# Performance work log

Measured on AMD Instinct MI355X. Metric: run time of the kernel, lower is better.

The kernel has to match this reference:

```python
import jax, jax.numpy as jnp
import numpy as np
from jax import lax

VOCAB, EMB, HID, MAXD, NCLS = 50000, 512, 512, 1024, 20
S, B = 512, 64

def setup_inputs() -> dict:
    key = jax.random.key(0)
    ks = jax.random.split(key, 16)
    sc = 0.05
    return {
        "inp": jax.random.randint(ks[0], (S, B), 0, VOCAB),
        "emb_table": jax.random.normal(ks[1], (VOCAB, EMB), jnp.float32) * sc,
        "c_l0": jax.random.normal(ks[2], (HID,), jnp.float32) * sc,
        "c_r0": jax.random.normal(ks[3], (HID,), jnp.float32) * sc,
        "W_l": jax.random.normal(ks[4], (HID, HID), jnp.float32) * sc,
        "b_l": jnp.zeros((HID,), jnp.float32),
        "W_r": jax.random.normal(ks[5], (HID, HID), jnp.float32) * sc,
        "b_r": jnp.zeros((HID,), jnp.float32),
        "W_sl": jax.random.normal(ks[6], (HID, EMB), jnp.float32) * sc,
        "b_sl": jnp.zeros((HID,), jnp.float32),
        "W_sr": jax.random.normal(ks[7], (EMB, HID), jnp.float32) * sc,  # emb_dim==hid_dim required by source
        "b_sr": jnp.zeros((EMB,), jnp.float32),
        "W_max": jax.random.normal(ks[8], (MAXD, 2 * HID + EMB), jnp.float32) * sc,
        "b_max": jnp.zeros((MAXD,), jnp.float32),
        "W_doc": jax.random.normal(ks[9], (NCLS, MAXD), jnp.float32) * sc,
        "b_doc": jnp.zeros((NCLS,), jnp.float32),
    }

def reference(inp, emb_table, c_l0, c_r0, W_l, b_l, W_r, b_r,
              W_sl, b_sl, W_sr, b_sr, W_max, b_max, W_doc, b_doc):
    # inp: [S, B] int; emb: [S, B, E]
    emb = emb_table[inp]
    # precomputed per-token projections (done once, outside the recurrence)
    emb_ls = jnp.einsum('sbe,he->sbh', emb, W_sl) + b_sl  # [S,B,H]
    emb_rs = jnp.einsum('sbe,he->sbh', emb, W_sr) + b_sr  # [S,B,H]

    def step(W, b):
        def f(c, e):  # c: [B,H], e: [B,H]
            c = jnp.tanh(c @ W.T + b + e)
            return c, c
        return f

    batch = inp.shape[1]
    c_l_init = jnp.broadcast_to(c_l0, (batch, HID))
    c_r_init = jnp.broadcast_to(c_r0, (batch, HID))
    _, c_ls = lax.scan(step(W_l, b_l), c_l_init, emb_ls)          # [S,B,H] left-to-right
    _, c_rs_rev = lax.scan(step(W_r, b_r), c_r_init, emb_rs[::-1])  # scanned right-to-left
    c_rs = c_rs_rev[::-1]                                          # re-aligned to positions

    cat = jnp.concatenate([c_ls, emb, c_rs], axis=2)               # [S,B,2H+E]
    y = jnp.tanh(jnp.einsum('sbc,mc->sbm', cat, W_max) + b_max)    # [S,B,M]
    y_max = jnp.max(y, axis=0)                                     # [B,M] max-pool over seq
    logits = y_max @ W_doc.T + b_doc                               # [B,C]
    return jax.nn.log_softmax(logits, axis=-1)
```

## Files before the change

kernel.cpp:

```cpp
#include <hip/hip_runtime.h>
#include <hip/hip_bf16.h>
#include <cstdint>
#include <cstddef>

#define SS   512
#define BB   64
#define EMBD 512
#define HIDD 512
#define MAXD 1024
#define NCLS 20
#define KCAT 1536
#define ROWS (SS*BB)

__device__ __forceinline__ uint16_t f2bf(float f) {
  uint32_t u = __float_as_uint(f);
  uint32_t r = u + 0x7fffu + ((u >> 16) & 1u);
  return (uint16_t)(r >> 16);
}
__device__ __forceinline__ float bf2f(uint32_t h) {
  return __uint_as_float(h << 16);
}
__device__ __forceinline__ uint32_t pk2(float a, float b) {
  return (uint32_t)f2bf(a) | ((uint32_t)f2bf(b) << 16);
}

__device__ __forceinline__ float fast_tanh(float x) {
  float ax = __builtin_fabsf(x);
  float e  = __builtin_amdgcn_exp2f(ax * -2.885390081777927f);
  float r  = (1.f - e) * __builtin_amdgcn_rcpf(1.f + e);
  return __builtin_copysignf(r, x);
}

#if defined(__has_builtin)
#if __has_builtin(__builtin_amdgcn_fdot2_f32_bf16)
#define USE_BF16_DOT2 1
#endif
#endif

#ifdef USE_BF16_DOT2
typedef __bf16 bf16x2_t __attribute__((ext_vector_type(2)));
__device__ __forceinline__ float dot2bf(uint32_t w, uint32_t c, float acc) {
  return __builtin_amdgcn_fdot2_f32_bf16(__builtin_bit_cast(bf16x2_t, w),
                                         __builtin_bit_cast(bf16x2_t, c), acc, false);
}
#else
__device__ __forceinline__ float dot2bf(uint32_t w, uint32_t c, float acc) {
  float w0 = __uint_as_float(w << 16);
  float w1 = __uint_as_float(w & 0xffff0000u);
  float c0 = __uint_as_float(c << 16);
  float c1 = __uint_as_float(c & 0xffff0000u);
  return fmaf(w1, c1, fmaf(w0, c0, acc));
}
#endif

__device__ __forceinline__ void gl_lds16(const void* g, void* l) {
  __builtin_amdgcn_global_load_lds((const __attribute__((address_space(1))) void*)g,
                                   (__attribute__((address_space(3))) void*)l,
                                   16, 0, 0);
}

typedef short v8s __attribute__((ext_vector_type(8)));
typedef float v4f __attribute__((ext_vector_type(4)));

__global__ __launch_bounds__(256) void prep_kernel(
    const int* __restrict__ inp, const float* __restrict__ table,
    const float* __restrict__ Wsl, const float* __restrict__ Wsr,
    const float* __restrict__ Wl,  const float* __restrict__ Wr,
    const float* __restrict__ Wmax,
    uint16_t* __restrict__ cat, uint16_t* __restrict__ wslb,
    uint16_t* __restrict__ wsrb, uint16_t* __restrict__ wlb,
    uint16_t* __restrict__ wrb, uint16_t* __restrict__ wmaxb)
{
  const int blk = blockIdx.x, t = threadIdx.x;
  if (blk < 8192) {
    const int r = blk * 4 + (t >> 6);
    const int lane = t & 63;
    const int token = inp[r];
    const float4* src = (const float4*)(table + (size_t)token * EMBD);
    uint16_t* dst = cat + (size_t)r * KCAT + 512;
#pragma unroll
    for (int p = 0; p < 2; ++p) {
      const int slot = lane + 64 * p;
      float4 v = src[slot];
      uint2 o;
      o.x = pk2(v.x, v.y);
      o.y = pk2(v.z, v.w);
      *(uint2*)(dst + slot * 4) = o;
    }
  } else {
    size_t flat = (size_t)(blk - 8192) * 2048 + (size_t)t * 8;
    const float* src; uint16_t* dst; size_t off;
    if (flat < 262144)       { src = Wsl;  dst = wslb;  off = flat; }
    else if (flat < 524288)  { src = Wsr;  dst = wsrb;  off = flat - 262144; }
    else if (flat < 786432)  { src = Wl;   dst = wlb;   off = flat - 524288; }
    else if (flat < 1048576) { src = Wr;   dst = wrb;   off = flat - 786432; }
    else                     { src = Wmax; dst = wmaxb; off = flat - 1048576; }
    float4 v0 = *(const float4*)(src + off);
    float4 v1 = *(const float4*)(src + off + 4);
    uint4 o;
    o.x = pk2(v0.x, v0.y); o.y = pk2(v0.z, v0.w);
    o.z = pk2(v1.x, v1.y); o.w = pk2(v1.z, v1.w);
    *(uint4*)(dst + off) = o;
  }
}

template<int MODE>
__global__ __launch_bounds__(256, 2) void gemm_kernel(
    const uint16_t* __restrict__ A, int lda, int K,
    const uint16_t* __restrict__ W0, const uint16_t* __restrict__ W1,
    const float* __restrict__ bias0, const float* __restrict__ bias1,
    uint16_t* __restrict__ outb, float* __restrict__ partial)
{
  __shared__ unsigned char smem[32768];
  uint16_t* lA = (uint16_t*)smem;
  uint16_t* lW = (uint16_t*)(smem + 16384);

  const int tid = threadIdx.x;
  const int mb = blockIdx.x, nb = blockIdx.y;
  const int m0 = mb * 128, n0 = nb * 128;

  const uint16_t* Wp = W0;
  const float* biasp = bias0;
  int nr0 = n0;
  if (MODE == 0 && n0 >= 512) { Wp = W1; biasp = bias1; nr0 = n0 - 512; }

  const int w = tid >> 6, lane = tid & 63;
  const int mw = w & 1, nw = w >> 1;

  v4f acc[4][4];
#pragma unroll
  for (int i = 0; i < 4; ++i)
#pragma unroll
    for (int j = 0; j < 4; ++j) {
      v4f z = {0.f, 0.f, 0.f, 0.f};
      acc[i][j] = z;
    }

  const int r_st = tid >> 3;
  const int u_st = tid & 7;

  for (int kk = 0; kk < K; kk += 64) {
    __syncthreads();
#pragma unroll
    for (int p = 0; p < 4; ++p) {
      const int r = p * 32 + r_st;
      gl_lds16(A + (size_t)(m0 + r) * lda + kk + u_st * 8, lA + (p * 256 + tid) * 8);
    }
#pragma unroll
    for (int p = 0; p < 4; ++p) {
      const int r = p * 32 + r_st;
      gl_lds16(Wp + (size_t)(nr0 + r) * K + kk + u_st * 8, lW + (p * 256 + tid) * 8);
    }
    __syncthreads();
#pragma unroll
    for (int ks = 0; ks < 2; ++ks) {
      v8s af[4], wf[4];
#pragma unroll
      for (int i = 0; i < 4; ++i)
        af[i] = *(const v8s*)&lA[(mw * 64 + i * 16 + (lane & 15)) * 64 + ks * 32 + (lane >> 4) * 8];
#pragma unroll
      for (int j = 0; j < 4; ++j)
        wf[j] = *(const v8s*)&lW[(nw * 64 + j * 16 + (lane & 15)) * 64 + ks * 32 + (lane >> 4) * 8];
#pragma unroll
      for (int i = 0; i < 4; ++i)
#pragma unroll
        for (int j = 0; j < 4; ++j)
          acc[i][j] = __builtin_amdgcn_mfma_f32_16x16x32_bf16(af[i], wf[j], acc[i][j], 0, 0, 0);
    }
  }

  __syncthreads();

  if (MODE == 0) {
#pragma unroll
    for (int i = 0; i < 4; ++i)
#pragma unroll
      for (int j = 0; j < 4; ++j) {
        const int nl = nw * 64 + j * 16 + (lane & 15);
        const float bv = biasp[nr0 + nl];
        const int colg = n0 + nl;
#pragma unroll
        for (int r = 0; r < 4; ++r) {
          const int rowg = m0 + mw * 64 + i * 16 + (lane >> 4) * 4 + r;
          outb[(size_t)rowg * 1024 + colg] = f2bf(acc[i][j][r] + bv);
        }
      }
  } else {
    float* lred = (float*)smem;
    if (mw == 1) {
#pragma unroll
      for (int i = 0; i < 4; ++i)
#pragma unroll
        for (int j = 0; j < 4; ++j) {
          const int nl = nw * 64 + j * 16 + (lane & 15);
          const float bv = biasp[nr0 + nl];
#pragma unroll
          for (int r = 0; r < 4; ++r) {
            const int bl = i * 16 + (lane >> 4) * 4 + r;
            lred[bl * 128 + nl] = fast_tanh(acc[i][j][r] + bv);
          }
        }
    }
    __syncthreads();
    if (mw == 0) {
#pragma unroll
      for (int i = 0; i < 4; ++i)
#pragma unroll
        for (int j = 0; j < 4; ++j) {
          const int nl = nw * 64 + j * 16 + (lane & 15);
          const float bv = biasp[nr0 + nl];
#pragma unroll
          for (int r = 0; r < 4; ++r) {
            const int bl = i * 16 + (lane >> 4) * 4 + r;
            const float v = fast_tanh(acc[i][j][r] + bv);
            partial[((size_t)mb * 64 + bl) * 1024 + n0 + nl] = fmaxf(v, lred[bl * 128 + nl]);
          }
        }
    }
  }
}

__global__ __launch_bounds__(512, 1) void scan_kernel(
    const uint16_t* __restrict__ ee,
    const uint16_t* __restrict__ wlb, const uint16_t* __restrict__ wrb,
    const float* __restrict__ bl, const float* __restrict__ br,
    const float* __restrict__ cl0, const float* __restrict__ cr0,
    uint16_t* __restrict__ cat,
    uint64_t* __restrict__ cbuf)
{
  const int tid = threadIdx.x;
  const int bid = blockIdx.x;
  const int b    = bid & 63;
  const int d    = (bid >> 6) & 1;
  const int half = bid >> 7;

  const int hp = tid & 127;
  const int kq = tid >> 7;

  __shared__ __align__(16) uint32_t cfull[256];
  __shared__ float2 part2[4 * 128];

  uint4 wA[16], wB[16];
  {
    const uint16_t* wsrc = (d ? wrb : wlb) + (size_t)(half * 256 + 2 * hp) * HIDD + kq * 128;
    const uint4* pA = (const uint4*)wsrc;
    const uint4* pB = (const uint4*)(wsrc + HIDD);
#pragma unroll
    for (int j = 0; j < 16; ++j) { wA[j] = pA[j]; wB[j] = pB[j]; }
  }
  if (tid < 256) {
    const float* c0v = d ? cr0 : cl0;
    float2 cv = ((const float2*)c0v)[tid];
    cfull[tid] = pk2(cv.x, cv.y);
  }
  float2 biasv = {0.f, 0.f};
  if (tid < 128) {
    const float* bvec = d ? br : bl;
    biasv = ((const float2*)bvec)[half * 128 + tid];
  }
  __syncthreads();

  const int fp = tid;
  const size_t ecol = (size_t)(d * 512 + half * 256 + 2 * fp);
  const int fcol = (d ? 1024 : 0) + half * 256 + 2 * fp;

  const int gj = tid - 128;
  const int pbid = bid ^ 128;

  uint32_t ep0 = 0, ep1 = 0;
  if (tid < 128) {
    const int s0i = d ? 511 : 0;
    const int s1i = d ? 510 : 1;
    ep0 = *(const uint32_t*)&ee[(size_t)(s0i * BB + b) * 1024 + ecol];
    ep1 = *(const uint32_t*)&ee[(size_t)(s1i * BB + b) * 1024 + ecol];
  }

  uint32_t prPrev = 0;
  int sPrev = -1;

  for (int i = 0; i < 512; ++i) {
    const int s = d ? (511 - i) : i;
    uint32_t ep2 = 0;
    if (tid < 128) {
      const int i2 = (i + 2) & 511;
      const int s2 = d ? (511 - i2) : i2;
      ep2 = *(const uint32_t*)&ee[(size_t)(s2 * BB + b) * 1024 + ecol];
      if (sPrev >= 0)
        *(uint32_t*)&cat[(size_t)(sPrev * BB + b) * KCAT + fcol] = prPrev;
    }

    {
      const uint32_t* cb_ = &cfull[kq * 64];
      float a0 = 0.f, a1 = 0.f, a2 = 0.f, a3 = 0.f;
#pragma unroll
      for (int j = 0; j < 16; ++j) {
        uint4 c4 = *(const uint4*)(cb_ + j * 4);
        a0 = dot2bf(wA[j].x, c4.x, a0); a2 = dot2bf(wB[j].x, c4.x, a2);
        a1 = dot2bf(wA[j].y, c4.y, a1); a3 = dot2bf(wB[j].y, c4.y, a3);
        a0 = dot2bf(wA[j].z, c4.z, a0); a2 = dot2bf(wB[j].z, c4.z, a2);
        a1 = dot2bf(wA[j].w, c4.w, a1); a3 = dot2bf(wB[j].w, c4.w, a3);
      }
      float2 pv; pv.x = a0 + a1; pv.y = a2 + a3;
      part2[kq * 128 + hp] = pv;
    }

    const uint64_t want = (uint64_t)(uint32_t)(i + 1);
    const uint64_t* slot = &cbuf[(size_t)(((i & 1) * 256 + pbid) * 128 + gj)];
    uint64_t vprobe = 0;
    if (tid >= 128 && tid < 256 && i != 511)
      vprobe = __hip_atomic_load(slot, __ATOMIC_RELAXED, __HIP_MEMORY_SCOPE_AGENT);

    __syncthreads();

    if (tid < 128) {
      float2 q0 = part2[fp];
      float2 q1 = part2[128 + fp];
      float2 q2 = part2[256 + fp];
      float2 q3 = part2[384 + fp];
      float s0 = ((q0.x + q1.x) + (q2.x + q3.x)) + biasv.x + bf2f(ep0 & 0xffffu);
      float s1 = ((q0.y + q1.y) + (q2.y + q3.y)) + biasv.y + bf2f(ep0 >> 16);
      uint32_t pr = pk2(fast_tanh(s0), fast_tanh(s1));
      if (i != 511) {
        uint64_t pkt = (want << 32) | (uint64_t)pr;
        __hip_atomic_store(&cbuf[(size_t)(((i & 1) * 256 + bid) * 128 + fp)],
                           pkt, __ATOMIC_RELAXED, __HIP_MEMORY_SCOPE_AGENT);
        cfull[half * 128 + fp] = pr;
        prPrev = pr; sPrev = s;
      } else {
        *(uint32_t*)&cat[(size_t)(s * BB + b) * KCAT + fcol] = pr;
      }
    } else if (tid < 256 && i != 511) {
      uint64_t v = vprobe;
      while ((v >> 32) != want) {
        v = __hip_atomic_load(slot, __ATOMIC_RELAXED, __HIP_MEMORY_SCOPE_AGENT);
        if ((v >> 32) == want) break;
        __builtin_amdgcn_s_sleep(1);
        v = __hip_atomic_load(slot, __ATOMIC_RELAXED, __HIP_MEMORY_SCOPE_AGENT);
      }
      cfull[(1 - half) * 128 + gj] = (uint32_t)v;
    }

    if (i == 511) break;
    __syncthreads();

    ep0 = ep1; ep1 = ep2;
  }
}

__global__ __launch_bounds__(256) void final_kernel(
    const float* __restrict__ partial, const float* __restrict__ Wdoc,
    const float* __restrict__ bdoc, float* __restrict__ out)
{
  const int b = blockIdx.x, t = threadIdx.x;
  __shared__ float ym[1024];
  __shared__ float lg[32];
  float m0 = -2.f, m1 = -2.f, m2 = -2.f, m3 = -2.f;
  for (int mg = 0; mg < 256; ++mg) {
    const float* p = partial + ((size_t)mg * 64 + b) * 1024;
    m0 = fmaxf(m0, p[t]);
    m1 = fmaxf(m1, p[t + 256]);
    m2 = fmaxf(m2, p[t + 512]);
    m3 = fmaxf(m3, p[t + 768]);
  }
  ym[t] = m0; ym[t + 256] = m1; ym[t + 512] = m2; ym[t + 768] = m3;
  __syncthreads();
  if (t < NCLS) {
    const float* wr = Wdoc + (size_t)t * 1024;
    float a0 = 0.f, a1 = 0.f, a2 = 0.f, a3 = 0.f;
    for (int n = 0; n < 1024; n += 4) {
      a0 = fmaf(ym[n], wr[n], a0);
      a1 = fmaf(ym[n + 1], wr[n + 1], a1);
      a2 = fmaf(ym[n + 2], wr[n + 2], a2);
      a3 = fmaf(ym[n + 3], wr[n + 3], a3);
    }
    lg[t] = (a0 + a1) + (a2 + a3) + bdoc[t];
  }
  __syncthreads();
  if (t < NCLS) {
    float mx = -1e30f;
    for (int c = 0; c < NCLS; ++c) mx = fmaxf(mx, lg[c]);
    float ssum = 0.f;
    for (int c = 0; c < NCLS; ++c) ssum += expf(lg[c] - mx);
    out[b * NCLS + t] = lg[t] - mx - logf(ssum);
  }
}

extern "C" void kernel_launch(void* const* d_in, const int* in_sizes, int n_in,
                              void* d_out, int out_size, void* d_ws, size_t ws_size,
                              hipStream_t stream) {
  const int*   inp   = (const int*)  d_in[0];
  const float* table = (const float*)d_in[1];
  const float* cl0   = (const float*)d_in[2];
  const float* cr0   = (const float*)d_in[3];
  const float* Wl    = (const float*)d_in[4];
  const float* bl    = (const float*)d_in[5];
  const float* Wr    = (const float*)d_in[6];
  const float* br    = (const float*)d_in[7];
  const float* Wsl   = (const float*)d_in[8];
  const float* bsl   = (const float*)d_in[9];
  const float* Wsr   = (const float*)d_in[10];
  const float* bsr   = (const float*)d_in[11];
  const float* Wmax  = (const float*)d_in[12];
  const float* bmax  = (const float*)d_in[13];
  const float* Wdoc  = (const float*)d_in[14];
  const float* bdoc  = (const float*)d_in[15];

  uint8_t* ws = (uint8_t*)d_ws;
  uint16_t* cat     = (uint16_t*)(ws);
  uint16_t* ee      = (uint16_t*)(ws + 100663296);
  float*    partial = (float*)   (ws + 167772160);
  uint16_t* wslb    = (uint16_t*)(ws + 234881024);
  uint16_t* wsrb    = (uint16_t*)(ws + 235405312);
  uint16_t* wmaxb   = (uint16_t*)(ws + 235929600);
  uint16_t* wlb     = (uint16_t*)(ws + 239075328);
  uint16_t* wrb     = (uint16_t*)(ws + 239599616);
  uint64_t* cbuf    = (uint64_t*)(ws + 167772160);

  prep_kernel<<<9472, 256, 0, stream>>>(inp, table, Wsl, Wsr, Wl, Wr, Wmax,
                                        cat, wslb, wsrb, wlb, wrb, wmaxb);
  gemm_kernel<0><<<dim3(256, 8), 256, 0, stream>>>(cat + 512, KCAT, 512, wslb, wsrb,
                                                   bsl, bsr, ee, nullptr);
  scan_kernel<<<256, 512, 0, stream>>>(ee, wlb, wrb, bl, br, cl0, cr0, cat, cbuf);
  gemm_kernel<1><<<dim3(256, 8), 256, 0, stream>>>(cat, KCAT, KCAT, wmaxb, nullptr,
                                                   bmax, nullptr, nullptr, partial);
  final_kernel<<<64, 256, 0, stream>>>(partial, Wdoc, bdoc, (float*)d_out);
}
```

Measured before the change: 1.117 ms.

## Let only remote-half waves poll peer state before their own matvec slice

The cross-block handoff of the peer block's half of the hidden state is restructured. Previously a dedicated group of threads polled for the peer's packet after the matvec and before the step barrier. Now each wave whose k-range covers the peer's half polls and writes those words into shared memory just before its own dot products. Waves on the local half start computing at once, and finalization moves to threads of the block's own half. This aims to overlap the inter-block latency with local work and drop a separate polling phase. In exchange it relies on wave-local shared-memory visibility and on duplicate writes from two waves being safe.

```diff
diff --git a/kernel.cpp b/kernel.cpp
--- a/kernel.cpp
+++ b/kernel.cpp
@@ -236,6 +236,7 @@
 
   const int hp = tid & 127;
   const int kq = tid >> 7;
+  const bool remote = (kq >> 1) != half;
 
   __shared__ __align__(16) uint32_t cfull[256];
   __shared__ float2 part2[4 * 128];
@@ -253,22 +254,27 @@
     float2 cv = ((const float2*)c0v)[tid];
     cfull[tid] = pk2(cv.x, cv.y);
   }
+
+  const int fbase = half * 256;
+  const unsigned ft = (unsigned)(tid - fbase);
+  const int fp = tid - fbase;
+
   float2 biasv = {0.f, 0.f};
-  if (tid < 128) {
+  if (ft < 128u) {
     const float* bvec = d ? br : bl;
-    biasv = ((const float2*)bvec)[half * 128 + tid];
+    biasv = ((const float2*)bvec)[half * 128 + fp];
   }
   __syncthreads();
 
-  const int fp = tid;
   const size_t ecol = (size_t)(d * 512 + half * 256 + 2 * fp);
   const int fcol = (d ? 1024 : 0) + half * 256 + 2 * fp;
 
-  const int gj = tid - 128;
-  const int pbid = bid ^ 128;
+  const int pslot = ((kq & 1) << 6) | (tid & 63);
+  const int cword = ((1 - half) << 7) | pslot;
+  const int pbid  = bid ^ 128;
 
   uint32_t ep0 = 0, ep1 = 0;
-  if (tid < 128) {
+  if (ft < 128u) {
     const int s0i = d ? 511 : 0;
     const int s1i = d ? 510 : 1;
     ep0 = *(const uint32_t*)&ee[(size_t)(s0i * BB + b) * 1024 + ecol];
@@ -281,12 +287,24 @@
   for (int i = 0; i < 512; ++i) {
     const int s = d ? (511 - i) : i;
     uint32_t ep2 = 0;
-    if (tid < 128) {
+    if (ft < 128u) {
       const int i2 = (i + 2) & 511;
       const int s2 = d ? (511 - i2) : i2;
       ep2 = *(const uint32_t*)&ee[(size_t)(s2 * BB + b) * 1024 + ecol];
       if (sPrev >= 0)
         *(uint32_t*)&cat[(size_t)(sPrev * BB + b) * KCAT + fcol] = prPrev;
+    }
+
+    if (remote && i != 0) {
+      const uint64_t want = (uint64_t)(uint32_t)i;
+      const uint64_t* slot = &cbuf[(size_t)(((((i & 1) ^ 1)) * 256 + pbid) * 128 + pslot)];
+      uint64_t v = __hip_atomic_load(slot, __ATOMIC_RELAXED, __HIP_MEMORY_SCOPE_AGENT);
+      while ((v >> 32) != want) {
+        __builtin_amdgcn_s_sleep(1);
+        v = __hip_atomic_load(slot, __ATOMIC_RELAXED, __HIP_MEMORY_SCOPE_AGENT);
+      }
+      cfull[cword] = (uint32_t)v;
+      asm volatile("s_waitcnt lgkmcnt(0)" ::: "memory");
     }
 
     {
@@ -304,15 +322,9 @@
       part2[kq * 128 + hp] = pv;
     }
 
-    const uint64_t want = (uint64_t)(uint32_t)(i + 1);
-    const uint64_t* slot = &cbuf[(size_t)(((i & 1) * 256 + pbid) * 128 + gj)];
-    uint64_t vprobe = 0;
-    if (tid >= 128 && tid < 256 && i != 511)
-      vprobe = __hip_atomic_load(slot, __ATOMIC_RELAXED, __HIP_MEMORY_SCOPE_AGENT);
-
     __syncthreads();
 
-    if (tid < 128) {
+    if (ft < 128u) {
       float2 q0 = part2[fp];
       float2 q1 = part2[128 + fp];
       float2 q2 = part2[256 + fp];
@@ -321,7 +333,7 @@
       float s1 = ((q0.y + q1.y) + (q2.y + q3.y)) + biasv.y + bf2f(ep0 >> 16);
       uint32_t pr = pk2(fast_tanh(s0), fast_tanh(s1));
       if (i != 511) {
-        uint64_t pkt = (want << 32) | (uint64_t)pr;
+        uint64_t pkt = ((uint64_t)(uint32_t)(i + 1) << 32) | (uint64_t)pr;
         __hip_atomic_store(&cbuf[(size_t)(((i & 1) * 256 + bid) * 128 + fp)],
                            pkt, __ATOMIC_RELAXED, __HIP_MEMORY_SCOPE_AGENT);
         cfull[half * 128 + fp] = pr;
@@ -329,15 +341,6 @@
       } else {
         *(uint32_t*)&cat[(size_t)(s * BB + b) * KCAT + fcol] = pr;
       }
-    } else if (tid < 256 && i != 511) {
-      uint64_t v = vprobe;
-      while ((v >> 32) != want) {
-        v = __hip_atomic_load(slot, __ATOMIC_RELAXED, __HIP_MEMORY_SCOPE_AGENT);
-        if ((v >> 32) == want) break;
-        __builtin_amdgcn_s_sleep(1);
-        v = __hip_atomic_load(slot, __ATOMIC_RELAXED, __HIP_MEMORY_SCOPE_AGENT);
-      }
-      cfull[(1 - half) * 128 + gj] = (uint32_t)v;
     }
 
     if (i == 511) break;
```

Measured after the change: 995.9 us. -10.8%, faster.

## Reduce scan partials with wave shuffles and double-buffer hidden state

Applied to the files above, without the earlier changes.

Each row's four K-quarter partial dot products now sit in adjacent lanes of one wavefront and are combined with xor-shuffles. This removes the shared-memory partial buffer and one block-wide barrier per recurrence step. The hidden-state vector is double-buffered in LDS with a rotated swizzle to avoid bank conflicts, so the next state can be written without racing readers. Finalize and poll duties now fall to specific lanes within every wave instead of whole waves, which may add divergence, and the weight registers are reorganised as scalar arrays.

```diff
diff --git a/kernel.cpp b/kernel.cpp
--- a/kernel.cpp
+++ b/kernel.cpp
@@ -233,42 +233,52 @@
   const int b    = bid & 63;
   const int d    = (bid >> 6) & 1;
   const int half = bid >> 7;
-
-  const int hp = tid & 127;
-  const int kq = tid >> 7;
-
-  __shared__ __align__(16) uint32_t cfull[256];
-  __shared__ float2 part2[4 * 128];
-
-  uint4 wA[16], wB[16];
+  const int lane = tid & 63;
+  const int w    = tid >> 6;
+
+  const int kq = lane & 3;
+  const int rp = (w << 4) | (lane >> 2);
+
+  __shared__ __align__(16) uint32_t cbuf2[2][256];
+
+  uint32_t wAa[64], wBa[64];
   {
-    const uint16_t* wsrc = (d ? wrb : wlb) + (size_t)(half * 256 + 2 * hp) * HIDD + kq * 128;
+    const uint16_t* wsrc = (d ? wrb : wlb) + (size_t)(half * 256 + 2 * rp) * HIDD + kq * 128;
     const uint4* pA = (const uint4*)wsrc;
     const uint4* pB = (const uint4*)(wsrc + HIDD);
 #pragma unroll
-    for (int j = 0; j < 16; ++j) { wA[j] = pA[j]; wB[j] = pB[j]; }
+    for (int j = 0; j < 16; ++j) {
+      uint4 qa = pA[j], qb = pB[j];
+      wAa[4 * j] = qa.x; wAa[4 * j + 1] = qa.y; wAa[4 * j + 2] = qa.z; wAa[4 * j + 3] = qa.w;
+      wBa[4 * j] = qb.x; wBa[4 * j + 1] = qb.y; wBa[4 * j + 2] = qb.z; wBa[4 * j + 3] = qb.w;
+    }
   }
   if (tid < 256) {
     const float* c0v = d ? cr0 : cl0;
-    float2 cv = ((const float2*)c0v)[tid];
-    cfull[tid] = pk2(cv.x, cv.y);
-  }
+    float2 cv0 = ((const float2*)c0v)[tid];
+    const int sw = (tid & ~63) | ((tid + ((tid >> 6) << 3)) & 63);
+    cbuf2[0][sw] = pk2(cv0.x, cv0.y);
+  }
+
+  const bool isFin  = (kq == 0);
+  const bool isPoll = (kq == 1);
+
   float2 biasv = {0.f, 0.f};
-  if (tid < 128) {
-    const float* bvec = d ? br : bl;
-    biasv = ((const float2*)bvec)[half * 128 + tid];
-  }
+  if (isFin) biasv = ((const float2*)(d ? br : bl))[half * 128 + rp];
+
+  const size_t ecol = (size_t)(d * 512 + half * 256 + 2 * rp);
+  const int fcol = (d ? 1024 : 0) + half * 256 + 2 * rp;
+
+  const int lw = (half << 7) | rp;
+  const int lwsw = (lw & ~63) | ((lw + ((lw >> 6) << 3)) & 63);
+  const int rw = ((1 - half) << 7) | rp;
+  const int rwsw = (rw & ~63) | ((rw + ((rw >> 6) << 3)) & 63);
+  const int pbid = bid ^ 128;
+
   __syncthreads();
 
-  const int fp = tid;
-  const size_t ecol = (size_t)(d * 512 + half * 256 + 2 * fp);
-  const int fcol = (d ? 1024 : 0) + half * 256 + 2 * fp;
-
-  const int gj = tid - 128;
-  const int pbid = bid ^ 128;
-
   uint32_t ep0 = 0, ep1 = 0;
-  if (tid < 128) {
+  if (isFin) {
     const int s0i = d ? 511 : 0;
     const int s1i = d ? 510 : 1;
     ep0 = *(const uint32_t*)&ee[(size_t)(s0i * BB + b) * 1024 + ecol];
@@ -281,7 +291,7 @@
   for (int i = 0; i < 512; ++i) {
     const int s = d ? (511 - i) : i;
     uint32_t ep2 = 0;
-    if (tid < 128) {
+    if (isFin) {
       const int i2 = (i + 2) & 511;
       const int s2 = d ? (511 - i2) : i2;
       ep2 = *(const uint32_t*)&ee[(size_t)(s2 * BB + b) * 1024 + ecol];
@@ -289,55 +299,55 @@
         *(uint32_t*)&cat[(size_t)(sPrev * BB + b) * KCAT + fcol] = prPrev;
     }
 
+    float se, so;
     {
-      const uint32_t* cb_ = &cfull[kq * 64];
+      const uint32_t* cb_ = &cbuf2[i & 1][kq * 64];
+      const int rot = kq << 3;
       float a0 = 0.f, a1 = 0.f, a2 = 0.f, a3 = 0.f;
 #pragma unroll
       for (int j = 0; j < 16; ++j) {
-        uint4 c4 = *(const uint4*)(cb_ + j * 4);
-        a0 = dot2bf(wA[j].x, c4.x, a0); a2 = dot2bf(wB[j].x, c4.x, a2);
-        a1 = dot2bf(wA[j].y, c4.y, a1); a3 = dot2bf(wB[j].y, c4.y, a3);
-        a0 = dot2bf(wA[j].z, c4.z, a0); a2 = dot2bf(wB[j].z, c4.z, a2);
-        a1 = dot2bf(wA[j].w, c4.w, a1); a3 = dot2bf(wB[j].w, c4.w, a3);
+        const int idx = ((j << 2) + rot) & 63;
+        uint4 c4 = *(const uint4*)(cb_ + idx);
+        a0 = dot2bf(wAa[4 * j],     c4.x, a0); a2 = dot2bf(wBa[4 * j],     c4.x, a2);
+        a1 = dot2bf(wAa[4 * j + 1], c4.y, a1); a3 = dot2bf(wBa[4 * j + 1], c4.y, a3);
+        a0 = dot2bf(wAa[4 * j + 2], c4.z, a0); a2 = dot2bf(wBa[4 * j + 2], c4.z, a2);
+        a1 = dot2bf(wAa[4 * j + 3], c4.w, a1); a3 = dot2bf(wBa[4 * j + 3], c4.w, a3);
       }
-      float2 pv; pv.x = a0 + a1; pv.y = a2 + a3;
-      part2[kq * 128 + hp] = pv;
+      se = a0 + a1; so = a2 + a3;
+      se += __shfl_xor(se, 1, 64); se += __shfl_xor(se, 2, 64);
+      so += __shfl_xor(so, 1, 64); so += __shfl_xor(so, 2, 64);
     }
 
     const uint64_t want = (uint64_t)(uint32_t)(i + 1);
-    const uint64_t* slot = &cbuf[(size_t)(((i & 1) * 256 + pbid) * 128 + gj)];
+    const uint64_t* slot = &cbuf[(size_t)(((i & 1) * 256 + pbid) * 128 + rp)];
     uint64_t vprobe = 0;
-    if (tid >= 128 && tid < 256 && i != 511)
+    if (isPoll && i != 511)
       vprobe = __hip_atomic_load(slot, __ATOMIC_RELAXED, __HIP_MEMORY_SCOPE_AGENT);
 
-    __syncthreads();
-
-    if (tid < 128) {
-      float2 q0 = part2[fp];
-      float2 q1 = part2[128 + fp];
-      float2 q2 = part2[256 + fp];
-      float2 q3 = part2[384 + fp];
-      float s0 = ((q0.x + q1.x) + (q2.x + q3.x)) + biasv.x + bf2f(ep0 & 0xffffu);
-      float s1 = ((q0.y + q1.y) + (q2.y + q3.y)) + biasv.y + bf2f(ep0 >> 16);
+    if (isFin) {
+      float s0 = se + biasv.x + bf2f(ep0 & 0xffffu);
+      float s1 = so + biasv.y + bf2f(ep0 >> 16);
       uint32_t pr = pk2(fast_tanh(s0), fast_tanh(s1));
       if (i != 511) {
         uint64_t pkt = (want << 32) | (uint64_t)pr;
-        __hip_atomic_store(&cbuf[(size_t)(((i & 1) * 256 + bid) * 128 + fp)],
+        __hip_atomic_store(&cbuf[(size_t)(((i & 1) * 256 + bid) * 128 + rp)],
                            pkt, __ATOMIC_RELAXED, __HIP_MEMORY_SCOPE_AGENT);
-        cfull[half * 128 + fp] = pr;
+        cbuf2[(i + 1) & 1][lwsw] = pr;
         prPrev = pr; sPrev = s;
       } else {
         *(uint32_t*)&cat[(size_t)(s * BB + b) * KCAT + fcol] = pr;
       }
-    } else if (tid < 256 && i != 511) {
+    }
+
+    __builtin_amdgcn_sched_barrier(0);
+
+    if (isPoll && i != 511) {
       uint64_t v = vprobe;
       while ((v >> 32) != want) {
-        v = __hip_atomic_load(slot, __ATOMIC_RELAXED, __HIP_MEMORY_SCOPE_AGENT);
-        if ((v >> 32) == want) break;
         __builtin_amdgcn_s_sleep(1);
         v = __hip_atomic_load(slot, __ATOMIC_RELAXED, __HIP_MEMORY_SCOPE_AGENT);
       }
-      cfull[(1 - half) * 128 + gj] = (uint32_t)v;
+      cbuf2[(i + 1) & 1][rwsw] = (uint32_t)v;
     }
 
     if (i == 511) break;
```

After: 1.363 ms. +22.0%, slower.
